# Optimization experiments

Measured on AMD Instinct MI355X. Metric: run time of the kernel, lower is better.

## Reference

```python
import jax, jax.numpy as jnp
import numpy as np

DEPTH = 17                 # levels of the complete binary tree
N = 2**DEPTH - 1           # 131071 nodes, BFS order: children of n are 2n+1, 2n+2
IN_DIM = 128
HID = 128
OUT = 128


def setup_inputs() -> dict:
    key = jax.random.key(0)
    ks = jax.random.split(key, 20)

    def lin_w(k, o, i):
        s = 1.0 / np.sqrt(i)
        return jax.random.uniform(k, (o, i), minval=-s, maxval=s, dtype=jnp.float32)

    def lin_b(k, o, i):
        s = 1.0 / np.sqrt(i)
        return jax.random.uniform(k, (o,), minval=-s, maxval=s, dtype=jnp.float32)

    inp = {"x": jax.random.normal(ks[0], (N, IN_DIM), dtype=jnp.float32)}
    # complete binary tree, parent -> child edges (row0=src/parent, row1=dst/child)
    child = np.arange(1, N)
    parent = (child - 1) // 2
    inp["edge_index"] = jnp.asarray(np.stack([parent, child]), dtype=jnp.int32)
    names = [("Wi", "bWi", IN_DIM), ("Ui", "bUi", HID),
             ("Wf", "bWf", IN_DIM), ("Uf", "bUf", HID),
             ("Wo", "bWo", IN_DIM), ("Uo", "bUo", HID),
             ("Wu", "bWu", IN_DIM), ("Uu", "bUu", HID)]
    ki = 1
    for wname, bname, idim in names:
        inp[wname] = lin_w(ks[ki], HID, idim)
        inp[bname] = lin_b(ks[ki + 1], HID, idim)
        ki += 2
    inp["Wp"] = lin_w(ks[17], OUT, HID)
    inp["bWp"] = lin_b(ks[18], OUT, HID)
    return inp


def reference(x, edge_index, Wi, bWi, Ui, bUi, Wf, bWf, Uf, bUf,
              Wo, bWo, Uo, bUo, Wu, bWu, Uu, bUu, Wp, bWp):
    # edge_index encodes the complete binary tree in BFS order (children of n
    # are 2n+1 and 2n+2), so the recursion batches exactly by tree level.
    # Precompute input-side gate projections for ALL nodes in 4 GEMMs
    # (equivalent to calling W_*(x[node]) per node in the torch recursion).
    xi = x @ Wi.T + bWi            # (N, H)
    xf = x @ Wf.T + bWf
    xo = x @ Wo.T + bWo
    xu = x @ Wu.T + bWu

    h_next = None  # hidden states of the level below (children)
    c_next = None
    for d in range(DEPTH - 1, -1, -1):   # bottom-up over tree levels
        s = 2**d - 1                     # first node index of level d
        cnt = 2**d                       # nodes at level d
        li, lf, lo, lu = xi[s:s + cnt], xf[s:s + cnt], xo[s:s + cnt], xu[s:s + cnt]
        if h_next is None:               # leaves: no children, h_sum = 0
            i = jax.nn.sigmoid(li)
            o = jax.nn.sigmoid(lo)
            u = jnp.tanh(lu)
            c = i * u
        else:
            # children of node s+k are at positions 2(s+k)+1, 2(s+k)+2: contiguous
            ch_h = h_next.reshape(cnt, 2, HID)
            ch_c = c_next.reshape(cnt, 2, HID)
            h_sum = ch_h.sum(axis=1)     # child-sum
            i = jax.nn.sigmoid(li + h_sum @ Ui.T + bUi)
            o = jax.nn.sigmoid(lo + h_sum @ Uo.T + bUo)
            u = jnp.tanh(lu + h_sum @ Uu.T + bUu)
            # per-child forget gates: sigmoid(W_f x + U_f h_k)
            f = jax.nn.sigmoid(lf[:, None, :] + jnp.einsum('nkh,gh->nkg', ch_h, Uf) + bUf)
            c = i * u + (f * ch_c).sum(axis=1)
        h = o * jnp.tanh(c)
        h_next, c_next = h, c

    h_root = h_next[0]                   # root node index 0
    # dropout is identity in eval mode
    return h_root @ Wp.T + bWp           # (OUT,)
```

## Files before the change

kernel.cpp:

```cpp
#include <hip/hip_runtime.h>
#include <hip/hip_bf16.h>


#define DEPTH 17
#define NTREE ((1 << DEPTH) - 1)
#define DIM 128
#define XSTR 136
#define HSTR 136
#define CSTR 132

typedef __attribute__((ext_vector_type(8))) short short8;
typedef __attribute__((ext_vector_type(4))) float float4v;

__device__ __forceinline__ float sigm(float v) {
    return __fdividef(1.0f, 1.0f + __expf(-v));
}
__device__ __forceinline__ float ftanh(float v) {
    v = fminf(15.0f, fmaxf(-15.0f, v));
    float e = __expf(2.0f * v);
    return __fdividef(e - 1.0f, e + 1.0f);
}

__device__ __forceinline__ unsigned short f2bf(float f) {
    union { float f; unsigned u; } a; a.f = f;
    unsigned u = a.u;
    return (unsigned short)((u + 0x7fffu + ((u >> 16) & 1u)) >> 16);
}
__device__ __forceinline__ float bf2f(unsigned short s) {
    union { unsigned u; float f; } a; a.u = ((unsigned)s) << 16;
    return a.f;
}

struct WPtrs {
    const float* W[4];  const float* U[4];
    const float* bW[4]; const float* bU[4];
};

__global__ __launch_bounds__(256) void prep_kernel(WPtrs p, unsigned short* __restrict__ Bsw,
                                                   float* __restrict__ biasWU, float* __restrict__ biasL) {
    int idx = blockIdx.x * 256 + threadIdx.x;
    int j = idx & 7;
    int lane = (idx >> 3) & 63;
    int g = (idx >> 9) & 3;
    int ks = (idx >> 11) & 7;
    int w = idx >> 14;
    int L = lane & 15, q = lane >> 4;
    int c = w * 16 + L;
    int k = ks * 32 + q * 8 + j;
    float v = (k < 128) ? p.W[g][c * 128 + k] * (g == 3 ? 1.0f : 0.5f)
                        : p.U[g][c * 128 + (k - 128)];
    Bsw[idx] = f2bf(v);
    if (idx < 512) {
        int gg = idx >> 7, cc = idx & 127;
        biasWU[idx] = p.bW[gg][cc] + p.bU[gg][cc];
        biasL[idx]  = p.bW[gg][cc];
    }
}

template <bool GCH>
__device__ __forceinline__ void internal_level(
    const unsigned short* xc,
    const unsigned short* hin_l, const float* cin_l,
    const unsigned short* __restrict__ hin_g, const float* __restrict__ cin_g, long cb,
    unsigned short* ho, float* co, int cnt,
    const short8 (&b)[32], const float* __restrict__ biasWU,
    int L, int q, int ch) {
    const int rows = 2 * cnt;
    const int mt = (rows + 15) >> 4;
    for (int mc = 0; mc < mt; mc += 2) {
        const int mm_n = (mt - mc >= 2) ? 2 : 1;
        float4v acc[2][4];
#pragma unroll
        for (int mm = 0; mm < 2; ++mm)
#pragma unroll
            for (int g = 0; g < 4; ++g) acc[mm][g] = (float4v){0.f, 0.f, 0.f, 0.f};

#pragma unroll
        for (int ks = 0; ks < 8; ++ks) {
            const int kk = ks * 32;
            short8 a[2];
#pragma unroll
            for (int mm = 0; mm < 2; ++mm) {
                if (mm < mm_n) {
                    if (kk < 128) {
                        int xr = 8 * (mc + mm) + (L >> 1);
                        if (xr >= cnt) xr = 0;
                        a[mm] = *(const short8*)(xc + xr * XSTR + kk + q * 8);
                    } else if (!GCH) {
                        a[mm] = *(const short8*)(hin_l + (16 * (mc + mm) + L) * HSTR + (kk - 128) + q * 8);
                    } else {
                        a[mm] = *(const short8*)(hin_g + (size_t)(cb + 16 * (mc + mm) + L) * DIM + (kk - 128) + q * 8);
                    }
                }
            }
#pragma unroll
            for (int g = 0; g < 4; ++g)
#pragma unroll
                for (int mm = 0; mm < 2; ++mm)
                    if (mm < mm_n)
                        acc[mm][g] = __builtin_amdgcn_mfma_f32_16x16x32_bf16(a[mm], b[ks * 4 + g], acc[mm][g], 0, 0, 0);
        }

#pragma unroll
        for (int mm = 0; mm < 2; ++mm)
#pragma unroll
            for (int e = 0; e < 2; ++e) {
                if (mm < mm_n) {
                    const int nl = 8 * (mc + mm) + 2 * q + e;
                    if (nl < cnt) {
                        const int r0 = 2 * e, r1 = 2 * e + 1;
                        float iv = sigm(acc[mm][0][r0] + acc[mm][0][r1] + biasWU[ch]);
                        float ov = sigm(acc[mm][1][r0] + acc[mm][1][r1] + biasWU[128 + ch]);
                        float uv = ftanh(acc[mm][2][r0] + acc[mm][2][r1] + biasWU[256 + ch]);
                        float fl = sigm(acc[mm][3][r0] + biasWU[384 + ch]);
                        float fr = sigm(acc[mm][3][r1] + biasWU[384 + ch]);
                        float cl, cr;
                        if (!GCH) {
                            cl = cin_l[(2 * nl) * CSTR + ch];
                            cr = cin_l[(2 * nl + 1) * CSTR + ch];
                        } else {
                            cl = cin_g[(size_t)(cb + 2 * nl) * DIM + ch];
                            cr = cin_g[(size_t)(cb + 2 * nl + 1) * DIM + ch];
                        }
                        float cv = iv * uv + fl * cl + fr * cr;
                        co[nl * CSTR + ch] = cv;
                        ho[nl * HSTR + ch] = f2bf(ov * ftanh(cv));
                    }
                }
            }
    }
}

__device__ __forceinline__ void leaf_level(
    const unsigned short* xc, unsigned short* ho, float* co,
    const short8 (&b)[32], const float* __restrict__ biasL,
    int L, int q, int ch) {
    float4v acc[2][3];
#pragma unroll
    for (int mm = 0; mm < 2; ++mm)
#pragma unroll
        for (int g = 0; g < 3; ++g) acc[mm][g] = (float4v){0.f, 0.f, 0.f, 0.f};
#pragma unroll
    for (int ks = 0; ks < 4; ++ks) {
        short8 a[2];
        a[0] = *(const short8*)(xc + L * XSTR + ks * 32 + q * 8);
        a[1] = *(const short8*)(xc + (16 + L) * XSTR + ks * 32 + q * 8);
#pragma unroll
        for (int g = 0; g < 3; ++g)
#pragma unroll
            for (int mm = 0; mm < 2; ++mm)
                acc[mm][g] = __builtin_amdgcn_mfma_f32_16x16x32_bf16(a[mm], b[ks * 4 + g], acc[mm][g], 0, 0, 0);
    }
#pragma unroll
    for (int mm = 0; mm < 2; ++mm)
#pragma unroll
        for (int r = 0; r < 4; ++r) {
            const int nl = 16 * mm + q * 4 + r;
            float iv = sigm(2.f * acc[mm][0][r] + biasL[ch]);
            float ov = sigm(2.f * acc[mm][1][r] + biasL[128 + ch]);
            float uv = ftanh(2.f * acc[mm][2][r] + biasL[256 + ch]);
            float cv = iv * uv;
            co[nl * CSTR + ch] = cv;
            ho[nl * HSTR + ch] = f2bf(ov * ftanh(cv));
        }
}

__global__ __launch_bounds__(512, 2) void k1_kernel(
    const float* __restrict__ x, const unsigned short* __restrict__ Bsw,
    const float* __restrict__ biasL, const float* __restrict__ biasWU,
    unsigned short* __restrict__ hbf, float* __restrict__ cbuf) {
    __shared__ __align__(16) unsigned short xs[63 * XSTR];
    __shared__ __align__(16) unsigned short hA[32 * HSTR];
    __shared__ __align__(16) unsigned short hB[16 * HSTR];
    __shared__ __align__(16) float cA[32 * CSTR];
    __shared__ __align__(16) float cB[16 * CSTR];

    const int tid = threadIdx.x;
    const int w = tid >> 6, lane = tid & 63, L = lane & 15, q = lane >> 4;
    const int ch = w * 16 + L;

    short8 b[32];
#pragma unroll
    for (int t = 0; t < 32; ++t)
        b[t] = *(const short8*)(Bsw + ((size_t)w << 14) + (t << 9) + lane * 8);

    for (int it = 0; it < 8; ++it) {
        const long t = (long)it * 256 + blockIdx.x;
        int xoff = 0;
#pragma unroll
        for (int l = 0; l < 6; ++l) {
            const int rows = 32 >> l;
            const long base = ((1 << (16 - l)) - 1) + t * rows;
            for (int i = tid; i < rows * 32; i += 512) {
                const int row = i >> 5, j = i & 31;
                float4 v = *(const float4*)(x + (size_t)(base + row) * DIM + j * 4);
                ushort4 o;
                o.x = f2bf(v.x); o.y = f2bf(v.y); o.z = f2bf(v.z); o.w = f2bf(v.w);
                *(ushort4*)(xs + (xoff + row) * XSTR + j * 4) = o;
            }
            xoff += rows;
        }
        __syncthreads();

        leaf_level(xs, hA, cA, b, biasL, L, q, ch);
        __syncthreads();

        const unsigned short* hin = hA;
        const float* cin = cA;
        xoff = 32;
#pragma unroll
        for (int l = 1; l < 6; ++l) {
            const int cnt = 32 >> l;
            unsigned short* ho = (l & 1) ? hB : hA;
            float* co = (l & 1) ? cB : cA;
            internal_level<false>(xs + xoff * XSTR, hin, cin, nullptr, nullptr, 0,
                                  ho, co, cnt, b, biasWU, L, q, ch);
            __syncthreads();
            hin = ho; cin = co; xoff += cnt;
        }

        const long ob = (long)((1 << 11) - 1) + t;
        if (tid < 32)
            *(float4*)(cbuf + (size_t)ob * DIM + tid * 4) = *(const float4*)(cin + tid * 4);
        else if (tid < 48)
            *(uint4*)(hbf + (size_t)ob * DIM + (tid - 32) * 8) = *(const uint4*)(hin + (tid - 32) * 8);
        __syncthreads();
    }
}

template <int C, int NL, bool PROJ>
__global__ __launch_bounds__(512, 2) void k23_kernel(
    const float* __restrict__ x, const unsigned short* __restrict__ Bsw,
    const float* __restrict__ biasWU, unsigned short* __restrict__ hbf,
    float* __restrict__ cbuf, int d0,
    const float* __restrict__ Wp, const float* __restrict__ bWp,
    float* __restrict__ out) {
    constexpr int TOTX = 2 * C - (C >> (NL - 1));
    constexpr int AR = (C < 16) ? 16 : C;
    __shared__ __align__(16) unsigned short xs[TOTX * XSTR];
    __shared__ __align__(16) unsigned short hA[AR * HSTR];
    __shared__ __align__(16) unsigned short hB[16 * HSTR];
    __shared__ __align__(16) float cA[AR * CSTR];
    __shared__ __align__(16) float cB[16 * CSTR];
    __shared__ float red[4][128];

    const int tid = threadIdx.x;
    const int w = tid >> 6, lane = tid & 63, L = lane & 15, q = lane >> 4;
    const int ch = w * 16 + L;

    short8 b[32];
#pragma unroll
    for (int t = 0; t < 32; ++t)
        b[t] = *(const short8*)(Bsw + ((size_t)w << 14) + (t << 9) + lane * 8);

    {
        int xoff = 0;
#pragma unroll
        for (int l = 0; l < NL; ++l) {
            const int rows = C >> l;
            const long base = ((1 << (d0 - l)) - 1) + (long)blockIdx.x * rows;
            for (int i = tid; i < rows * 32; i += 512) {
                const int row = i >> 5, j = i & 31;
                float4 v = *(const float4*)(x + (size_t)(base + row) * DIM + j * 4);
                ushort4 o;
                o.x = f2bf(v.x); o.y = f2bf(v.y); o.z = f2bf(v.z); o.w = f2bf(v.w);
                *(ushort4*)(xs + (xoff + row) * XSTR + j * 4) = o;
            }
            xoff += rows;
        }
    }
    __syncthreads();

    const long cb = ((1 << (d0 + 1)) - 1) + (long)blockIdx.x * (2 * C);
    internal_level<true>(xs, nullptr, nullptr, hbf, cbuf, cb,
                         hA, cA, C, b, biasWU, L, q, ch);
    __syncthreads();

    const unsigned short* hin = hA;
    const float* cin = cA;
    int xoff = C;
#pragma unroll
    for (int l = 1; l < NL; ++l) {
        const int cnt = C >> l;
        unsigned short* ho = (l & 1) ? hB : hA;
        float* co = (l & 1) ? cB : cA;
        internal_level<false>(xs + xoff * XSTR, hin, cin, nullptr, nullptr, 0,
                              ho, co, cnt, b, biasWU, L, q, ch);
        __syncthreads();
        hin = ho; cin = co; xoff += cnt;
    }

    if (PROJ) {
        const int o = tid & 127, sg = tid >> 7;
        float pacc = 0.f;
#pragma unroll
        for (int jj = 0; jj < 8; ++jj) {
            const int k = sg * 32 + jj * 4;
            float4 wv = *(const float4*)(Wp + o * DIM + k);
            pacc += bf2f(hin[k]) * wv.x + bf2f(hin[k + 1]) * wv.y +
                    bf2f(hin[k + 2]) * wv.z + bf2f(hin[k + 3]) * wv.w;
        }
        red[sg][o] = pacc;
        __syncthreads();
        if (tid < 128) out[tid] = bWp[tid] + red[0][tid] + red[1][tid] + red[2][tid] + red[3][tid];
    } else {
        const long ob = ((1 << (d0 - (NL - 1))) - 1) + (long)blockIdx.x;
        if (tid < 32)
            *(float4*)(cbuf + (size_t)ob * DIM + tid * 4) = *(const float4*)(cin + tid * 4);
        else if (tid < 48)
            *(uint4*)(hbf + (size_t)ob * DIM + (tid - 32) * 8) = *(const uint4*)(hin + (tid - 32) * 8);
    }
}

extern "C" void kernel_launch(void* const* d_in, const int* in_sizes, int n_in,
                              void* d_out, int out_size, void* d_ws, size_t ws_size,
                              hipStream_t stream) {
    const float* x   = (const float*)d_in[0];
    const float* Wi  = (const float*)d_in[2];  const float* bWi = (const float*)d_in[3];
    const float* Ui  = (const float*)d_in[4];  const float* bUi = (const float*)d_in[5];
    const float* Wf  = (const float*)d_in[6];  const float* bWf = (const float*)d_in[7];
    const float* Uf  = (const float*)d_in[8];  const float* bUf = (const float*)d_in[9];
    const float* Wo  = (const float*)d_in[10]; const float* bWo = (const float*)d_in[11];
    const float* Uo  = (const float*)d_in[12]; const float* bUo = (const float*)d_in[13];
    const float* Wu  = (const float*)d_in[14]; const float* bWu = (const float*)d_in[15];
    const float* Uu  = (const float*)d_in[16]; const float* bUu = (const float*)d_in[17];
    const float* Wp  = (const float*)d_in[18]; const float* bWp = (const float*)d_in[19];

    unsigned short* Bsw = (unsigned short*)d_ws;
    float* biasWU = (float*)(Bsw + 131072);
    float* biasL  = biasWU + 512;
    float* cbuf   = biasL + 512;
    unsigned short* hbf = (unsigned short*)(cbuf + (size_t)NTREE * DIM);

    WPtrs p;
    p.W[0] = Wi; p.W[1] = Wo; p.W[2] = Wu; p.W[3] = Wf;
    p.U[0] = Ui; p.U[1] = Uo; p.U[2] = Uu; p.U[3] = Uf;
    p.bW[0] = bWi; p.bW[1] = bWo; p.bW[2] = bWu; p.bW[3] = bWf;
    p.bU[0] = bUi; p.bU[1] = bUo; p.bU[2] = bUu; p.bU[3] = bUf;

    prep_kernel<<<512, 256, 0, stream>>>(p, Bsw, biasWU, biasL);

    k1_kernel<<<256, 512, 0, stream>>>(x, Bsw, biasL, biasWU, hbf, cbuf);
    k23_kernel<32, 6, false><<<32, 512, 0, stream>>>(x, Bsw, biasWU, hbf, cbuf, 10,
                                                     nullptr, nullptr, nullptr);
    k23_kernel<16, 5, true><<<1, 512, 0, stream>>>(x, Bsw, biasWU, hbf, cbuf, 4,
                                                   Wp, bWp, (float*)d_out);
}
```

Measured before the change: 255.4 us.

## Pre-convert x to bf16, prefetch next tile in registers, write last level directly

Adds a separate kernel that converts x to bf16 once, so k1 and k23 load bf16 rows directly instead of converting fp32 on the fly. k1 now register-prefetches the next iteration's 63 x rows while the current tree levels compute, overlapping global loads with MFMA work. The final level of each subtree writes h/c straight to global memory, removing the copy-out step and a barrier, and the workspace shrinks cbuf/hbf to 4096 rows. LDS strides change from 136 to 132, which may alter bank conflicts. The extra conversion pass adds a full read and write of x.

Result: slower. 357.4 us (+39.9%).

```diff
diff --git a/kernel.cpp b/kernel.cpp
--- a/kernel.cpp
+++ b/kernel.cpp
@@ -5,8 +5,8 @@
 #define DEPTH 17
 #define NTREE ((1 << DEPTH) - 1)
 #define DIM 128
-#define XSTR 136
-#define HSTR 136
+#define XSTR 132
+#define HSTR 132
 #define CSTR 132
 
 typedef __attribute__((ext_vector_type(8))) short short8;
@@ -57,12 +57,24 @@
     }
 }
 
+__global__ __launch_bounds__(256) void convx_kernel(const float* __restrict__ x,
+                                                    unsigned short* __restrict__ xbf, int n4) {
+    int i = blockIdx.x * 256 + threadIdx.x;
+    int stride = gridDim.x * 256;
+    for (; i < n4; i += stride) {
+        float4 v = ((const float4*)x)[i];
+        ushort4 o;
+        o.x = f2bf(v.x); o.y = f2bf(v.y); o.z = f2bf(v.z); o.w = f2bf(v.w);
+        ((ushort4*)xbf)[i] = o;
+    }
+}
+
 template <bool GCH>
 __device__ __forceinline__ void internal_level(
     const unsigned short* xc,
     const unsigned short* hin_l, const float* cin_l,
     const unsigned short* __restrict__ hin_g, const float* __restrict__ cin_g, long cb,
-    unsigned short* ho, float* co, int cnt,
+    unsigned short* ho, int ho_str, float* co, int co_str, int cnt,
     const short8 (&b)[32], const float* __restrict__ biasWU,
     int L, int q, int ch) {
     const int rows = 2 * cnt;
@@ -123,8 +135,8 @@
                             cr = cin_g[(size_t)(cb + 2 * nl + 1) * DIM + ch];
                         }
                         float cv = iv * uv + fl * cl + fr * cr;
-                        co[nl * CSTR + ch] = cv;
-                        ho[nl * HSTR + ch] = f2bf(ov * ftanh(cv));
+                        co[nl * co_str + ch] = cv;
+                        ho[nl * ho_str + ch] = f2bf(ov * ftanh(cv));
                     }
                 }
             }
@@ -166,7 +178,7 @@
 }
 
 __global__ __launch_bounds__(512, 2) void k1_kernel(
-    const float* __restrict__ x, const unsigned short* __restrict__ Bsw,
+    const unsigned short* __restrict__ xbf, const unsigned short* __restrict__ Bsw,
     const float* __restrict__ biasL, const float* __restrict__ biasWU,
     unsigned short* __restrict__ hbf, float* __restrict__ cbuf) {
     __shared__ __align__(16) unsigned short xs[63 * XSTR];
@@ -184,53 +196,76 @@
     for (int t = 0; t < 32; ++t)
         b[t] = *(const short8*)(Bsw + ((size_t)w << 14) + (t << 9) + lane * 8);
 
+    uint4 pf[2];
+    {
+        const long t0 = blockIdx.x;
+#pragma unroll
+        for (int k = 0; k < 2; ++k) {
+            const int i = tid + 512 * k;
+            if (i < 1008) {
+                const int row = i >> 4, g = i & 15;
+                const int l = __clz(63 - row) - 26;
+                const long node = ((1L << (16 - l)) - 1) + t0 * (32 >> l) + (row - (64 - (64 >> l)));
+                pf[k] = *(const uint4*)(xbf + (size_t)node * DIM + g * 8);
+            }
+        }
+    }
+
     for (int it = 0; it < 8; ++it) {
         const long t = (long)it * 256 + blockIdx.x;
-        int xoff = 0;
-#pragma unroll
-        for (int l = 0; l < 6; ++l) {
-            const int rows = 32 >> l;
-            const long base = ((1 << (16 - l)) - 1) + t * rows;
-            for (int i = tid; i < rows * 32; i += 512) {
-                const int row = i >> 5, j = i & 31;
-                float4 v = *(const float4*)(x + (size_t)(base + row) * DIM + j * 4);
-                ushort4 o;
-                o.x = f2bf(v.x); o.y = f2bf(v.y); o.z = f2bf(v.z); o.w = f2bf(v.w);
-                *(ushort4*)(xs + (xoff + row) * XSTR + j * 4) = o;
-            }
-            xoff += rows;
+
+#pragma unroll
+        for (int k = 0; k < 2; ++k) {
+            const int i = tid + 512 * k;
+            if (i < 1008) {
+                const int row = i >> 4, g = i & 15;
+                *(uint4*)(xs + row * XSTR + g * 8) = pf[k];
+            }
         }
         __syncthreads();
+
+        if (it < 7) {
+            const long tn = t + 256;
+#pragma unroll
+            for (int k = 0; k < 2; ++k) {
+                const int i = tid + 512 * k;
+                if (i < 1008) {
+                    const int row = i >> 4, g = i & 15;
+                    const int l = __clz(63 - row) - 26;
+                    const long node = ((1L << (16 - l)) - 1) + tn * (32 >> l) + (row - (64 - (64 >> l)));
+                    pf[k] = *(const uint4*)(xbf + (size_t)node * DIM + g * 8);
+                }
+            }
+        }
 
         leaf_level(xs, hA, cA, b, biasL, L, q, ch);
         __syncthreads();
 
         const unsigned short* hin = hA;
         const float* cin = cA;
-        xoff = 32;
-#pragma unroll
-        for (int l = 1; l < 6; ++l) {
+        int xoff = 32;
+#pragma unroll
+        for (int l = 1; l < 5; ++l) {
             const int cnt = 32 >> l;
             unsigned short* ho = (l & 1) ? hB : hA;
             float* co = (l & 1) ? cB : cA;
             internal_level<false>(xs + xoff * XSTR, hin, cin, nullptr, nullptr, 0,
-                                  ho, co, cnt, b, biasWU, L, q, ch);
+                                  ho, HSTR, co, CSTR, cnt, b, biasWU, L, q, ch);
             __syncthreads();
             hin = ho; cin = co; xoff += cnt;
         }
 
-        const long ob = (long)((1 << 11) - 1) + t;
-        if (tid < 32)
-            *(float4*)(cbuf + (size_t)ob * DIM + tid * 4) = *(const float4*)(cin + tid * 4);
-        else if (tid < 48)
-            *(uint4*)(hbf + (size_t)ob * DIM + (tid - 32) * 8) = *(const uint4*)(hin + (tid - 32) * 8);
+        const long ob = 2047 + t;
+        internal_level<false>(xs + 62 * XSTR, hin, cin, nullptr, nullptr, 0,
+                              hbf + (size_t)ob * DIM, DIM,
+                              cbuf + (size_t)ob * DIM, DIM, 1, b, biasWU, L, q, ch);
         __syncthreads();
     }
 }
 
 template <int C, int NL, bool PROJ>
 __global__ __launch_bounds__(512, 2) void k23_kernel(
-    const float* __restrict__ x, const unsigned short* __restrict__ Bsw,
+    const unsigned short* __restrict__ xbf, const unsigned short* __restrict__ Bsw,
     const float* __restrict__ biasWU, unsigned short* __restrict__ hbf,
     float* __restrict__ cbuf, int d0,
     const float* __restrict__ Wp, const float* __restrict__ bWp,
@@ -259,12 +294,10 @@
         for (int l = 0; l < NL; ++l) {
             const int rows = C >> l;
             const long base = ((1 << (d0 - l)) - 1) + (long)blockIdx.x * rows;
-            for (int i = tid; i < rows * 32; i += 512) {
-                const int row = i >> 5, j = i & 31;
-                float4 v = *(const float4*)(x + (size_t)(base + row) * DIM + j * 4);
-                ushort4 o;
-                o.x = f2bf(v.x); o.y = f2bf(v.y); o.z = f2bf(v.z); o.w = f2bf(v.w);
-                *(ushort4*)(xs + (xoff + row) * XSTR + j * 4) = o;
+            for (int i = tid; i < rows * 16; i += 512) {
+                const int row = i >> 4, g = i & 15;
+                *(uint4*)(xs + (xoff + row) * XSTR + g * 8) =
+                    *(const uint4*)(xbf + (size_t)(base + row) * DIM + g * 8);
             }
             xoff += rows;
         }
@@ -273,7 +306,7 @@
 
     const long cb = ((1 << (d0 + 1)) - 1) + (long)blockIdx.x * (2 * C);
     internal_level<true>(xs, nullptr, nullptr, hbf, cbuf, cb,
-                         hA, cA, C, b, biasWU, L, q, ch);
+                         hA, HSTR, cA, CSTR, C, b, biasWU, L, q, ch);
     __syncthreads();
 
     const unsigned short* hin = hA;
@@ -282,12 +315,20 @@
 #pragma unroll
     for (int l = 1; l < NL; ++l) {
         const int cnt = C >> l;
-        unsigned short* ho = (l & 1) ? hB : hA;
-        float* co = (l & 1) ? cB : cA;
-        internal_level<false>(xs + xoff * XSTR, hin, cin, nullptr, nullptr, 0,
-                              ho, co, cnt, b, biasWU, L, q, ch);
-        __syncthreads();
-        hin = ho; cin = co; xoff += cnt;
+        if (!PROJ && l == NL - 1) {
+            const long ob = ((1 << (d0 - (NL - 1))) - 1) + (long)blockIdx.x;
+            internal_level<false>(xs + xoff * XSTR, hin, cin, nullptr, nullptr, 0,
+                                  hbf + (size_t)ob * DIM, DIM,
+                                  cbuf + (size_t)ob * DIM, DIM, cnt, b, biasWU, L, q, ch);
+        } else {
+            unsigned short* ho = (l & 1) ? hB : hA;
+            float* co = (l & 1) ? cB : cA;
+            internal_level<false>(xs + xoff * XSTR, hin, cin, nullptr, nullptr, 0,
+                                  ho, HSTR, co, CSTR, cnt, b, biasWU, L, q, ch);
+            __syncthreads();
+            hin = ho; cin = co;
+        }
+        xoff += cnt;
     }
 
     if (PROJ) {
@@ -303,12 +344,6 @@
         red[sg][o] = pacc;
         __syncthreads();
         if (tid < 128) out[tid] = bWp[tid] + red[0][tid] + red[1][tid] + red[2][tid] + red[3][tid];
-    } else {
-        const long ob = ((1 << (d0 - (NL - 1))) - 1) + (long)blockIdx.x;
-        if (tid < 32)
-            *(float4*)(cbuf + (size_t)ob * DIM + tid * 4) = *(const float4*)(cin + tid * 4);
-        else if (tid < 48)
-            *(uint4*)(hbf + (size_t)ob * DIM + (tid - 32) * 8) = *(const uint4*)(hin + (tid - 32) * 8);
     }
 }
 
@@ -330,7 +365,8 @@
     float* biasWU = (float*)(Bsw + 131072);
     float* biasL  = biasWU + 512;
     float* cbuf   = biasL + 512;
-    unsigned short* hbf = (unsigned short*)(cbuf + (size_t)NTREE * DIM);
+    unsigned short* hbf = (unsigned short*)(cbuf + (size_t)4096 * DIM);
+    unsigned short* xbf = hbf + (size_t)4096 * DIM;
 
     WPtrs p;
     p.W[0] = Wi; p.W[1] = Wo; p.W[2] = Wu; p.W[3] = Wf;
@@ -339,10 +375,11 @@
     p.bU[0] = bUi; p.bU[1] = bUo; p.bU[2] = bUu; p.bU[3] = bUf;
 
     prep_kernel<<<512, 256, 0, stream>>>(p, Bsw, biasWU, biasL);
-
-    k1_kernel<<<256, 512, 0, stream>>>(x, Bsw, biasL, biasWU, hbf, cbuf);
-    k23_kernel<32, 6, false><<<32, 512, 0, stream>>>(x, Bsw, biasWU, hbf, cbuf, 10,
+    convx_kernel<<<4096, 256, 0, stream>>>(x, xbf, NTREE * 32);
+
+    k1_kernel<<<256, 512, 0, stream>>>(xbf, Bsw, biasL, biasWU, hbf, cbuf);
+    k23_kernel<32, 6, false><<<32, 512, 0, stream>>>(xbf, Bsw, biasWU, hbf, cbuf, 10,
                                                      nullptr, nullptr, nullptr);
-    k23_kernel<16, 5, true><<<1, 512, 0, stream>>>(x, Bsw, biasWU, hbf, cbuf, 4,
+    k23_kernel<16, 5, true><<<1, 512, 0, stream>>>(xbf, Bsw, biasWU, hbf, cbuf, 4,
                                                    Wp, bWp, (float*)d_out);
 }
```
